# Optimization experiments

Hardware: AMD Instinct MI355X
Metric: run time of the kernel (lower is better)

Reference implementation:

```python
import jax, jax.numpy as jnp
import numpy as np

ALPHA = 0.25
GAMMA = 2.0
COST_MASK = 1.0
COST_DICE = 1.0


def setup_inputs() -> dict:
    key = jax.random.key(0)
    k1, k2 = jax.random.split(key)
    B, N, M, H, W = 4, 100, 20, 256, 256
    outputs = jax.random.normal(k1, (B, N, H, W), dtype=jnp.float32)
    # binary target masks; threshold ensures every mask is non-empty so the
    # data-dependent tgt_ids truncation in the original is a no-op
    targets = (jax.random.uniform(k2, (B, M, H, W)) > 0.7).astype(jnp.float32)
    return {"outputs": outputs, "targets": targets}


def _cost_matrix(out_mask, tgt_mask):
    # out_mask: [N, HW] logits, tgt_mask: [M, HW] binary
    hw = out_mask.shape[1]
    prob = jax.nn.sigmoid(out_mask)
    # BCE-with-logits: target=1 -> softplus(-x); target=0 -> softplus(x)
    bce_pos = jax.nn.softplus(-out_mask)
    bce_neg = jax.nn.softplus(out_mask)
    focal_pos = ALPHA * (1.0 - prob) ** GAMMA * bce_pos            # [N, HW]
    focal_neg = (1.0 - ALPHA) * prob ** GAMMA * bce_neg            # [N, HW]
    cost_mask = (jnp.einsum('nc,mc->nm', focal_pos, tgt_mask)
                 + jnp.einsum('nc,mc->nm', focal_neg, 1.0 - tgt_mask)) / hw
    # dice cost
    numerator = 2.0 * jnp.einsum('nc,mc->nm', prob, tgt_mask)
    denominator = prob.sum(-1)[:, None] + tgt_mask.sum(-1)[None, :]
    cost_dice = 1.0 - (numerator + 1.0) / (denominator + 1.0)
    return COST_MASK * cost_mask + COST_DICE * cost_dice           # [N, M]


def reference(outputs, targets):
    B, N, H, W = outputs.shape
    M = targets.shape[1]
    out_flat = outputs.reshape(B, N, H * W)
    tgt_flat = targets.reshape(B, M, H * W)
    # vmap over batch: per-image [N, M] cost matrix fed to Hungarian on CPU
    C = jax.vmap(_cost_matrix)(out_flat, tgt_flat)  # [B, N, M]
    return C
```

## Files before the change

### kernel.cpp

```cpp
#include <hip/hip_runtime.h>
#include <math.h>

#define BB 4
#define NN 100
#define MM 20
#define HWPIX 65536
#define NT 7
#define GSEG 64
#define BLKPX (HWPIX / GSEG)
#define ROUNDPX 256
#define LDSROW 260
#define PSLOTS 728

typedef float f32x4 __attribute__((ext_vector_type(4)));
typedef short bf16x8 __attribute__((ext_vector_type(8)));

__global__ __launch_bounds__(256) void pack_kernel(
    const float* __restrict__ tgt,
    unsigned int* __restrict__ masks)
{
    const int b = blockIdx.x >> 6;
    const int c = ((blockIdx.x & 63) << 10) | (threadIdx.x << 2);
    const float* tb = tgt + (size_t)b * MM * HWPIX + c;

    unsigned int mk0 = 0, mk1 = 0, mk2 = 0, mk3 = 0;
#pragma unroll
    for (int m = 0; m < MM; ++m) {
        const f32x4 t = *(const f32x4*)(tb + (size_t)m * HWPIX);
        mk0 |= (t.x > 0.5f) ? (1u << m) : 0u;
        mk1 |= (t.y > 0.5f) ? (1u << m) : 0u;
        mk2 |= (t.z > 0.5f) ? (1u << m) : 0u;
        mk3 |= (t.w > 0.5f) ? (1u << m) : 0u;
    }
    uint4 v; v.x = mk0; v.y = mk1; v.z = mk2; v.w = mk3;
    *(uint4*)(masks + (size_t)b * HWPIX + c) = v;
}

__global__ __launch_bounds__(256, 4) void cost_mfma_kernel(
    const float* __restrict__ out,
    const unsigned int* __restrict__ masks,
    float* __restrict__ part)
{
    const int g    = blockIdx.x & (GSEG - 1);
    const int nt   = (blockIdx.x >> 6) % NT;
    const int b    = blockIdx.x / (GSEG * NT);
    const int tid  = threadIdx.x;
    const int w    = tid >> 6;
    const int lane = tid & 63;
    const int lrow = lane & 15;
    const int quad = lane >> 4;

    __shared__ __align__(16) float lds[16 * LDSROW];

    const unsigned int* mrow = masks + (size_t)b * HWPIX;
    const int colbase = g * BLKPX;

    f32x4 d1a = {0,0,0,0}, d1b = {0,0,0,0};
    f32x4 d2a = {0,0,0,0}, d2b = {0,0,0,0};
    f32x4 d3a = {0,0,0,0}, d3b = {0,0,0,0};
    float sfn = 0.f, sp = 0.f;

    bf16x8 ones;
#pragma unroll
    for (int j = 0; j < 8; ++j) ones[j] = (short)0x3F80;

#define EVALJ(XV, MK, J)                                                    \
    {                                                                       \
        const float x_   = (XV);                                            \
        const float ex_  = __builtin_amdgcn_exp2f(x_ * 1.44269504f);        \
        const float ope_ = 1.f + ex_;                                       \
        const float bn_  = 0.69314718f * __builtin_amdgcn_logf(ope_);       \
        const float bp_  = bn_ - x_;                                        \
        const float p_   = ex_ * __builtin_amdgcn_rcpf(ope_);               \
        const float om_  = 1.f - p_;                                        \
        const float fpv_ = (0.25f * om_) * (om_ * bp_);                     \
        const float fnv_ = (0.75f * p_) * (p_ * bn_);                      \
        sfn += fnv_; sp += p_;                                              \
        fdv[J] = (short)__builtin_bit_cast(unsigned short, (__bf16)(fpv_ - fnv_)); \
        fpr[J] = (short)__builtin_bit_cast(unsigned short, (__bf16)p_);     \
        const unsigned s_ = (MK) >> lrow;                                   \
        t0[J]  = (short)((s_ & 1u) * 0x3F80u);                              \
        t1[J]  = (short)(((s_ >> 16) & 1u) * 0x3F80u);                      \
    }

    for (int r = 0; r < 4; ++r) {
#pragma unroll
        for (int rr = 0; rr < 4; ++rr) {
            const int rs = w * 4 + rr;
            const int gn = min(nt * 16 + rs, NN - 1);
            const float* gp = out + (size_t)(b * NN + gn) * HWPIX
                            + colbase + r * ROUNDPX + lane * 4;
            __builtin_amdgcn_global_load_lds(gp, &lds[rs * LDSROW], 16, 0, 0);
        }
        __syncthreads();

#pragma unroll
        for (int c = 0; c < 2; ++c) {
            const int lcol = w * 64 + c * 32 + quad * 8;
            const float* xp = &lds[lrow * LDSROW + lcol];
            const f32x4 xaC = *(const f32x4*)xp;
            const f32x4 xbC = *(const f32x4*)(xp + 4);
            const unsigned* mp = mrow + colbase + r * ROUNDPX + lcol;
            const uint4 qaC = *(const uint4*)mp;
            const uint4 qbC = *(const uint4*)(mp + 4);

            bf16x8 fdv, fpr, t0, t1;
            EVALJ(xaC.x, qaC.x, 0)
            EVALJ(xaC.y, qaC.y, 1)
            EVALJ(xaC.z, qaC.z, 2)
            EVALJ(xaC.w, qaC.w, 3)
            EVALJ(xbC.x, qbC.x, 4)
            EVALJ(xbC.y, qbC.y, 5)
            EVALJ(xbC.z, qbC.z, 6)
            EVALJ(xbC.w, qbC.w, 7)

            d1a = __builtin_amdgcn_mfma_f32_16x16x32_bf16(fdv,  t0, d1a, 0, 0, 0);
            d2a = __builtin_amdgcn_mfma_f32_16x16x32_bf16(fpr,  t0, d2a, 0, 0, 0);
            d3a = __builtin_amdgcn_mfma_f32_16x16x32_bf16(ones, t0, d3a, 0, 0, 0);
            d1b = __builtin_amdgcn_mfma_f32_16x16x32_bf16(fdv,  t1, d1b, 0, 0, 0);
            d2b = __builtin_amdgcn_mfma_f32_16x16x32_bf16(fpr,  t1, d2b, 0, 0, 0);
            d3b = __builtin_amdgcn_mfma_f32_16x16x32_bf16(ones, t1, d3b, 0, 0, 0);
        }
        __syncthreads();
    }
#undef EVALJ

    sfn += __shfl_xor(sfn, 16, 64); sfn += __shfl_xor(sfn, 32, 64);
    sp  += __shfl_xor(sp,  16, 64); sp  += __shfl_xor(sp,  32, 64);

    float* lw = lds + w * PSLOTS;
#pragma unroll
    for (int r = 0; r < 4; ++r) {
        const int nl = quad * 4 + r;
        lw[nl * 44 + lrow]      = d1a[r];
        lw[nl * 44 + 20 + lrow] = d2a[r];
        if (lrow < 4) {
            lw[nl * 44 + 16 + lrow] = d1b[r];
            lw[nl * 44 + 36 + lrow] = d2b[r];
        }
    }
    if (lane < 16) {
        lw[lrow * 44 + 40] = sfn;
        lw[lrow * 44 + 41] = sp;
        lw[lrow * 44 + 42] = 0.f;
        lw[lrow * 44 + 43] = 0.f;
    }
    if (quad == 0) {
        lw[704 + lrow] = d3a[0];
        if (lrow < 4) lw[720 + lrow] = d3b[0];
    }
    if (quad == 1 && lrow < 4) lw[724 + lrow] = 0.f;
    __syncthreads();

    float* pout = part + (size_t)blockIdx.x * PSLOTS;
    for (int idx = tid; idx < PSLOTS; idx += 256)
        pout[idx] = lds[idx] + lds[PSLOTS + idx] + lds[2 * PSLOTS + idx]
                  + lds[3 * PSLOTS + idx];
}

__global__ __launch_bounds__(256) void combine_kernel(
    const float* __restrict__ part,
    float* __restrict__ C)
{
    const int bn = blockIdx.x;
    const int b  = bn / NN;
    const int n  = bn - b * NN;
    const int nt = n >> 4, nl = n & 15;
    const float* pbase = part + (size_t)((b * NT + nt) * GSEG) * PSLOTS;

    const int t  = threadIdx.x;
    const int s  = t & 63;
    const int gp = t >> 6;

    float acc = 0.f;
    if (s < 44) {
        const int off = nl * 44 + s;
#pragma unroll
        for (int gg = 0; gg < 16; ++gg)
            acc += pbase[(size_t)(gp * 16 + gg) * PSLOTS + off];
    } else {
        const int off = 704 + (s - 44);
#pragma unroll
        for (int gg = 0; gg < 16; ++gg)
            acc += pbase[(size_t)(gp * 16 + gg) * PSLOTS + off];
    }

    __shared__ float r1[4][64];
    r1[gp][s] = acc;
    __syncthreads();

    if (t < MM) {
        const int m = t;
        float D1 = 0.f, D2 = 0.f, SFN = 0.f, SP = 0.f, TS = 0.f;
#pragma unroll
        for (int g4 = 0; g4 < 4; ++g4) {
            D1  += r1[g4][m];
            D2  += r1[g4][20 + m];
            SFN += r1[g4][40];
            SP  += r1[g4][41];
            TS  += r1[g4][44 + m];
        }
        const float cost_mask = (SFN + D1) * (1.f / (float)HWPIX);
        const float den  = SP + TS;
        const float dice = 1.f - (2.f * D2 + 1.f) / (den + 1.f);
        C[bn * MM + m] = cost_mask + dice;
    }
}

extern "C" void kernel_launch(void* const* d_in, const int* in_sizes, int n_in,
                              void* d_out, int out_size, void* d_ws, size_t ws_size,
                              hipStream_t stream)
{
    const float* outp = (const float*)d_in[0];
    const float* tgtp = (const float*)d_in[1];
    float* C = (float*)d_out;

    char* ws = (char*)d_ws;
    unsigned int* masks = (unsigned int*)ws;
    float* part = (float*)(ws + (size_t)BB * HWPIX * sizeof(unsigned int));

    pack_kernel<<<BB * 64, 256, 0, stream>>>(tgtp, masks);
    cost_mfma_kernel<<<BB * NT * GSEG, 256, 0, stream>>>(outp, masks, part);
    combine_kernel<<<BB * NN, 256, 0, stream>>>(part, C);
}
```

Measured before the change: 177.4 us.

## Double-buffer LDS staging of logits to overlap global loads with compute

Splits the LDS tile into two buffers and prefetches the next round's logit rows via global_load_lds while the current round is evaluated. Each round waits only on the previous stage with an explicit s_waitcnt vmcnt before a raw s_barrier, instead of a full __syncthreads after the loads. This aims to hide global-memory latency behind the transcendental and MFMA work. The cost is doubled staging LDS, which may reduce occupancy, and a hand-counted vmcnt that could break if the compiler reorders the other global loads.

```diff
diff --git a/kernel.cpp b/kernel.cpp
--- a/kernel.cpp
+++ b/kernel.cpp
@@ -50,10 +50,13 @@
     const int lrow = lane & 15;
     const int quad = lane >> 4;
 
-    __shared__ __align__(16) float lds[16 * LDSROW];
+    __shared__ __align__(16) float lds[2][16 * LDSROW];
 
     const unsigned int* mrow = masks + (size_t)b * HWPIX;
     const int colbase = g * BLKPX;
+
+    const int rs0 = w * 4;
+    const float* gsrc[1];
 
     f32x4 d1a = {0,0,0,0}, d1b = {0,0,0,0};
     f32x4 d2a = {0,0,0,0}, d2b = {0,0,0,0};
@@ -83,21 +86,33 @@
         t1[J]  = (short)(((s_ >> 16) & 1u) * 0x3F80u);                      \
     }
 
+#define STAGE(R, BUFI)                                                      \
+    {                                                                       \
+        _Pragma("unroll")                                                   \
+        for (int rr = 0; rr < 4; ++rr) {                                    \
+            const int rs = rs0 + rr;                                        \
+            const int gn = min(nt * 16 + rs, NN - 1);                       \
+            const float* gp = out + (size_t)(b * NN + gn) * HWPIX           \
+                            + colbase + (R) * ROUNDPX + lane * 4;           \
+            __builtin_amdgcn_global_load_lds(gp, &lds[BUFI][rs * LDSROW],   \
+                                             16, 0, 0);                     \
+        }                                                                   \
+    }
+
+    STAGE(0, 0)
+
+#pragma unroll
     for (int r = 0; r < 4; ++r) {
-#pragma unroll
-        for (int rr = 0; rr < 4; ++rr) {
-            const int rs = w * 4 + rr;
-            const int gn = min(nt * 16 + rs, NN - 1);
-            const float* gp = out + (size_t)(b * NN + gn) * HWPIX
-                            + colbase + r * ROUNDPX + lane * 4;
-            __builtin_amdgcn_global_load_lds(gp, &lds[rs * LDSROW], 16, 0, 0);
-        }
-        __syncthreads();
+        if (r < 3) STAGE(r + 1, (r + 1) & 1)
+
+        if (r < 3) asm volatile("s_waitcnt vmcnt(4)" ::: "memory");
+        else       asm volatile("s_waitcnt vmcnt(0)" ::: "memory");
+        __builtin_amdgcn_s_barrier();
 
 #pragma unroll
         for (int c = 0; c < 2; ++c) {
             const int lcol = w * 64 + c * 32 + quad * 8;
-            const float* xp = &lds[lrow * LDSROW + lcol];
+            const float* xp = &lds[r & 1][lrow * LDSROW + lcol];
             const f32x4 xaC = *(const f32x4*)xp;
             const f32x4 xbC = *(const f32x4*)(xp + 4);
             const unsigned* mp = mrow + colbase + r * ROUNDPX + lcol;
@@ -121,14 +136,15 @@
             d2b = __builtin_amdgcn_mfma_f32_16x16x32_bf16(fpr,  t1, d2b, 0, 0, 0);
             d3b = __builtin_amdgcn_mfma_f32_16x16x32_bf16(ones, t1, d3b, 0, 0, 0);
         }
-        __syncthreads();
+        __builtin_amdgcn_s_barrier();
     }
 #undef EVALJ
+#undef STAGE
 
     sfn += __shfl_xor(sfn, 16, 64); sfn += __shfl_xor(sfn, 32, 64);
     sp  += __shfl_xor(sp,  16, 64); sp  += __shfl_xor(sp,  32, 64);
 
-    float* lw = lds + w * PSLOTS;
+    float* lw = &lds[0][0] + w * PSLOTS;
 #pragma unroll
     for (int r = 0; r < 4; ++r) {
         const int nl = quad * 4 + r;
@@ -152,10 +168,11 @@
     if (quad == 1 && lrow < 4) lw[724 + lrow] = 0.f;
     __syncthreads();
 
+    const float* lr = &lds[0][0];
     float* pout = part + (size_t)blockIdx.x * PSLOTS;
     for (int idx = tid; idx < PSLOTS; idx += 256)
-        pout[idx] = lds[idx] + lds[PSLOTS + idx] + lds[2 * PSLOTS + idx]
-                  + lds[3 * PSLOTS + idx];
+        pout[idx] = lr[idx] + lr[PSLOTS + idx] + lr[2 * PSLOTS + idx]
+                  + lr[3 * PSLOTS + idx];
 }
 
 __global__ __launch_bounds__(256) void combine_kernel(
```

Result: slower. 181.2 us (+2.2%).
